# Performance work log

Hardware: AMD Instinct MI355X
Metric: run time of the kernel (lower is better)

## Reference

```python
import jax, jax.numpy as jnp
import numpy as np
import math

E = 2048         # n_embd
H = 16           # num query head pairs (num_heads)
HKV = 8          # num_kv_heads
NREP = H // HKV  # 2
HD = E // H // 2 # head_dim = 64
DEPTH = 12
LAMBDA_INIT = 0.8 - 0.6 * math.exp(-0.3 * DEPTH)
EPS = 1e-6


def setup_inputs() -> dict:
    key = jax.random.key(0)
    ks = jax.random.split(key, 10)
    s = lambda fan_in: 1.0 / np.sqrt(fan_in)
    return {
        "x": jax.random.normal(ks[0], (2, 2048, E), jnp.float32),
        "Wq": jax.random.normal(ks[1], (E, E), jnp.float32) * s(E),
        "Wk": jax.random.normal(ks[2], (E, E // NREP), jnp.float32) * s(E),
        "Wv": jax.random.normal(ks[3], (E, E // NREP), jnp.float32) * s(E),
        "Wo": jax.random.normal(ks[4], (E, E), jnp.float32) * s(E),
        "lam_q1": jax.random.normal(ks[5], (HD,), jnp.float32) * 0.1,
        "lam_k1": jax.random.normal(ks[6], (HD,), jnp.float32) * 0.1,
        "lam_q2": jax.random.normal(ks[7], (HD,), jnp.float32) * 0.1,
        "lam_k2": jax.random.normal(ks[8], (HD,), jnp.float32) * 0.1,
        "g": jnp.ones((2 * HD,), jnp.float32),  # RMSNorm weight
    }


def _rotary(x, cos, sin):
    # x: [B, T, nh, HD]; cos/sin: [T, HD//2]
    d = x.shape[-1] // 2
    x1, x2 = x[..., :d], x[..., d:]
    c = cos[None, :, None, :]
    si = sin[None, :, None, :]
    return jnp.concatenate([x1 * c + x2 * si, -x1 * si + x2 * c], axis=-1)


def reference(x, Wq, Wk, Wv, Wo, lam_q1, lam_k1, lam_q2, lam_k2, g):
    B, T, _ = x.shape
    q = (x @ Wq).reshape(B, T, 2 * H, HD)
    k = (x @ Wk).reshape(B, T, 2 * HKV, HD)
    v = (x @ Wv).reshape(B, T, HKV, 2 * HD)

    inv_freq = 1.0 / (10000.0 ** (jnp.arange(0, HD, 2, dtype=jnp.float32) / HD))
    freqs = jnp.arange(T, dtype=jnp.float32)[:, None] * inv_freq[None, :]
    cos, sin = jnp.cos(freqs), jnp.sin(freqs)
    q = _rotary(q, cos, sin)
    k = _rotary(k, cos, sin)

    q = jnp.transpose(q, (0, 2, 1, 3)) * (HD ** -0.5)   # [B, 2H, T, HD]
    k = jnp.repeat(jnp.transpose(k, (0, 2, 1, 3)), NREP, axis=1)  # [B, 2H, T, HD]
    v = jnp.repeat(jnp.transpose(v, (0, 2, 1, 3)), NREP, axis=1)  # [B, H, T, 2HD]

    scores = jnp.einsum('bhtd,bhsd->bhts', q, k)
    scores = jnp.nan_to_num(scores)
    mask = jnp.triu(jnp.full((T, T), -jnp.inf, scores.dtype), 1)
    scores = scores + mask
    p = jax.nn.softmax(scores.astype(jnp.float32), axis=-1).astype(scores.dtype)

    lam1 = jnp.exp(jnp.sum(lam_q1 * lam_k1))
    lam2 = jnp.exp(jnp.sum(lam_q2 * lam_k2))
    lam = lam1 - lam2 + LAMBDA_INIT

    p = p.reshape(B, H, 2, T, T)
    diff = p[:, :, 0] - lam * p[:, :, 1]               # [B, H, T, T]
    attn = jnp.einsum('bhts,bhsd->bhtd', diff, v)      # [B, H, T, 2HD]

    # RMSNorm over last dim (2*HD)
    attn = attn * jax.lax.rsqrt(jnp.mean(attn * attn, axis=-1, keepdims=True) + EPS) * g
    attn = attn * (1.0 - LAMBDA_INIT)
    attn = jnp.transpose(attn, (0, 2, 1, 3)).reshape(B, T, E)
    return attn @ Wo
```

## Files before the change

### kernel.cpp

```cpp
#include <hip/hip_runtime.h>

#define T_SEQ 2048

typedef __bf16 bf16x8 __attribute__((ext_vector_type(8)));
typedef float f32x4 __attribute__((ext_vector_type(4)));
typedef unsigned short u16;

__device__ __forceinline__ u16 f2b(float f) {
  unsigned u = __float_as_uint(f);
  unsigned r = 0x7fffu + ((u >> 16) & 1u);
  return (u16)((u + r) >> 16);
}
__device__ __forceinline__ float b2f(u16 v) {
  return __uint_as_float(((unsigned)v) << 16);
}
__device__ __forceinline__ f32x4 mfma16(bf16x8 a, bf16x8 b, f32x4 c) {
  return __builtin_amdgcn_mfma_f32_16x16x32_bf16(a, b, c, 0, 0, 0);
}
__device__ __forceinline__ unsigned pkhi(float lo, float hi) {
  return __builtin_amdgcn_perm(__float_as_uint(hi), __float_as_uint(lo), 0x07060302u);
}
#if defined(__has_builtin)
#if __has_builtin(__builtin_amdgcn_exp2f)
#define HAVE_RAW_EXP2 1
#endif
#endif
__device__ __forceinline__ float exp2r(float x) {
#ifdef HAVE_RAW_EXP2
  return __builtin_amdgcn_exp2f(x);
#else
  float r;
  asm("v_exp_f32 %0, %1" : "=v"(r) : "v"(x));
  return r;
#endif
}
__device__ __forceinline__ void glds16(const void* g, void* s) {
  __builtin_amdgcn_global_load_lds(
      (const __attribute__((address_space(1))) void*)(uintptr_t)g,
      (__attribute__((address_space(3))) void*)(unsigned)(uintptr_t)s, 16, 0, 0);
}

__global__ void lam_kernel(const float* __restrict__ q1, const float* __restrict__ k1,
                           const float* __restrict__ q2, const float* __restrict__ k2,
                           float* __restrict__ outp) {
  int l = threadIdx.x;
  float a = q1[l] * k1[l];
  float c = q2[l] * k2[l];
  #pragma unroll
  for (int off = 32; off > 0; off >>= 1) {
    a += __shfl_down(a, off);
    c += __shfl_down(c, off);
  }
  if (l == 0) outp[0] = expf(a) - expf(c) + 0.7836057665316244f;
}

__global__ __launch_bounds__(256) void convert_kernel(const float* __restrict__ in,
                                                      u16* __restrict__ outp, int n) {
  int i = (blockIdx.x * 256 + threadIdx.x) * 4;
  if (i >= n) return;
  float4 v = *(const float4*)(in + i);
  ushort4 pk;
  pk.x = f2b(v.x); pk.y = f2b(v.y); pk.z = f2b(v.z); pk.w = f2b(v.w);
  *(ushort4*)(outp + i) = pk;
}

__global__ __launch_bounds__(256) void transposeW_kernel(const float* __restrict__ Wq,
                                                         const float* __restrict__ Wk,
                                                         const float* __restrict__ Wv,
                                                         const float* __restrict__ Wo,
                                                         u16* __restrict__ outp) {
  __shared__ float tile[32][33];
  const int ro0 = blockIdx.y * 32;
  const int r0 = blockIdx.x * 32;
  const float* src; int C, cbase;
  if (ro0 < 2048)      { src = Wq; C = 2048; cbase = 0; }
  else if (ro0 < 3072) { src = Wk; C = 1024; cbase = 2048; }
  else if (ro0 < 4096) { src = Wv; C = 1024; cbase = 3072; }
  else                 { src = Wo; C = 2048; cbase = 4096; }
  const int cs0 = ro0 - cbase;
  const int tx = threadIdx.x & 31, ty = threadIdx.x >> 5;
  #pragma unroll
  for (int k2 = 0; k2 < 4; k2++)
    tile[ty * 4 + k2][tx] = src[(size_t)(r0 + ty * 4 + k2) * C + cs0 + tx];
  __syncthreads();
  #pragma unroll
  for (int k2 = 0; k2 < 4; k2++)
    outp[(size_t)(ro0 + ty * 4 + k2) * 2048 + r0 + tx] = f2b(tile[tx][ty * 4 + k2]);
}

template <bool OUT_BF16>
__global__ __launch_bounds__(256) void gemm128_kernel(const u16* __restrict__ A,
                                                      const u16* __restrict__ BT,
                                                      void* __restrict__ C, int N, int K) {
  __shared__ alignas(16) u16 As[128 * 64];
  __shared__ alignas(16) u16 Bs[128 * 64];
  const int tid = threadIdx.x, w = tid >> 6, lane = tid & 63;
  const int l15 = lane & 15, quad = lane >> 4;
  const int m0 = blockIdx.y * 128, n0 = blockIdx.x * 128;
  const int wm = (w >> 1) * 64, wn = (w & 1) * 64;
  const int lr = lane >> 3, slot = lane & 7, csw = slot ^ lr;
  f32x4 acc[4][4];
  #pragma unroll
  for (int mt = 0; mt < 4; mt++)
    #pragma unroll
    for (int nt = 0; nt < 4; nt++) acc[mt][nt] = (f32x4){0.f, 0.f, 0.f, 0.f};
  const u16* Ag = A + (size_t)(m0 + w * 32 + lr) * K + csw * 8;
  const u16* Bg = BT + (size_t)(n0 + w * 32 + lr) * K + csw * 8;
  u16* Asd = As + (w * 32) * 64;
  u16* Bsd = Bs + (w * 32) * 64;
  for (int kt = 0; kt < K; kt += 64) {
    #pragma unroll
    for (int i = 0; i < 4; i++) {
      glds16(Ag + kt + (size_t)(i * 8) * K, Asd + i * 512);
      glds16(Bg + kt + (size_t)(i * 8) * K, Bsd + i * 512);
    }
    __syncthreads();
    #pragma unroll
    for (int kk = 0; kk < 2; kk++) {
      bf16x8 am[4], bn[4];
      #pragma unroll
      for (int t = 0; t < 4; t++) {
        const int ra = wm + t * 16 + l15;
        am[t] = *(const bf16x8*)&As[ra * 64 + (((kk * 4 + quad) ^ (ra & 7)) << 3)];
        const int rb = wn + t * 16 + l15;
        bn[t] = *(const bf16x8*)&Bs[rb * 64 + (((kk * 4 + quad) ^ (rb & 7)) << 3)];
      }
      #pragma unroll
      for (int mt = 0; mt < 4; mt++)
        #pragma unroll
        for (int nt = 0; nt < 4; nt++) acc[mt][nt] = mfma16(am[mt], bn[nt], acc[mt][nt]);
    }
    __syncthreads();
  }
  const int row = m0 + wm + quad * 4;
  #pragma unroll
  for (int mt = 0; mt < 4; mt++) {
    #pragma unroll
    for (int nt = 0; nt < 4; nt++) {
      const int col = n0 + wn + nt * 16 + l15;
      #pragma unroll
      for (int rr = 0; rr < 4; rr++) {
        if (OUT_BF16)
          ((u16*)C)[(size_t)(row + mt * 16 + rr) * N + col] = f2b(acc[mt][nt][rr]);
        else
          ((float*)C)[(size_t)(row + mt * 16 + rr) * N + col] = acc[mt][nt][rr];
      }
    }
  }
}

#define STAGE_HALF(TILE, ROLE, BUF)                                                     \
  do {                                                                                  \
    const u16* sp_ = ((ROLE) == 0 || (ROLE) == 3 ? Ag : Bg) +                           \
                     (size_t)((ROLE) >= 2 ? 128 : 0) * K + (size_t)(TILE) * 64;         \
    u16* dp_ = ((ROLE) == 0 || (ROLE) == 3 ? &As[BUF][0] : &Bs[BUF][0]) +               \
               (((ROLE) >= 2 ? 128 : 0) + w * 8) * 64;                                  \
    glds16(sp_, dp_);                                                                   \
    glds16(sp_ + (size_t)64 * K, dp_ + 4096);                                           \
  } while (0)

#define PHASE(I, J, BUF, NEWA, NEWB, BN, STILE, SROLE, SBUF, DOVM)                      \
  do {                                                                                  \
    if (NEWA) {                                                                         \
      _Pragma("unroll") for (int u_ = 0; u_ < 4; u_++) {                                \
        const int ar_ = ((I) * 4 + u_) * 32 + wm * 16 + l15;                            \
        _Pragma("unroll") for (int kk_ = 0; kk_ < 2; kk_++)                             \
            am[u_][kk_] = *(const bf16x8*)&As[BUF][ar_ * 64 +                           \
                              (((kk_ * 4 + quad) ^ (ar_ & 7)) << 3)];                   \
      }                                                                                 \
    }                                                                                   \
    if (NEWB) {                                                                         \
      _Pragma("unroll") for (int v_ = 0; v_ < 2; v_++) {                                \
        const int br_ = ((J) * 2 + v_) * 64 + wn * 16 + l15;                            \
        _Pragma("unroll") for (int kk_ = 0; kk_ < 2; kk_++)                             \
            BN[v_][kk_] = *(const bf16x8*)&Bs[BUF][br_ * 64 +                           \
                              (((kk_ * 4 + quad) ^ (br_ & 7)) << 3)];                   \
      }                                                                                 \
    }                                                                                   \
    STAGE_HALF(STILE, SROLE, SBUF);                                                     \
    __builtin_amdgcn_s_barrier();                                                       \
    asm volatile("s_waitcnt lgkmcnt(0)" ::: "memory");                                  \
    __builtin_amdgcn_sched_barrier(0);                                                  \
    __builtin_amdgcn_s_setprio(1);                                                      \
    _Pragma("unroll") for (int u_ = 0; u_ < 4; u_++)                                    \
        _Pragma("unroll") for (int v_ = 0; v_ < 2; v_++) {                              \
      acc[(I) * 4 + u_][(J) * 2 + v_] =                                                 \
          mfma16(am[u_][0], BN[v_][0], acc[(I) * 4 + u_][(J) * 2 + v_]);                \
      acc[(I) * 4 + u_][(J) * 2 + v_] =                                                 \
          mfma16(am[u_][1], BN[v_][1], acc[(I) * 4 + u_][(J) * 2 + v_]);                \
    }                                                                                   \
    __builtin_amdgcn_s_setprio(0);                                                      \
    if (DOVM) asm volatile("s_waitcnt vmcnt(6)" ::: "memory");                          \
    __builtin_amdgcn_s_barrier();                                                       \
  } while (0)

__global__ __launch_bounds__(512, 2) void gemm256_kernel(const u16* __restrict__ A,
                                                         const u16* __restrict__ BT,
                                                         u16* __restrict__ C, int N, int K) {
  __shared__ alignas(16) u16 As[2][256 * 64];
  __shared__ alignas(16) u16 Bs[2][256 * 64];
  const int tid = threadIdx.x, w = tid >> 6, lane = tid & 63;
  const int l15 = lane & 15, quad = lane >> 4;
  const int wm = w >> 2, wn = w & 3;
  const int lr = lane >> 3, slot = lane & 7, csw = slot ^ lr;
  const int m0 = blockIdx.y * 256, n0 = blockIdx.x * 256;
  const int nkt = K >> 6;

  f32x4 acc[8][4];
  #pragma unroll
  for (int r = 0; r < 8; r++)
    #pragma unroll
    for (int s = 0; s < 4; s++) acc[r][s] = (f32x4){0.f, 0.f, 0.f, 0.f};

  const u16* Ag = A + (size_t)(m0 + w * 8 + lr) * K + csw * 8;
  const u16* Bg = BT + (size_t)(n0 + w * 8 + lr) * K + csw * 8;

  bf16x8 am[4][2], bn0[2][2], bn1[2][2];

  STAGE_HALF(0, 0, 0); STAGE_HALF(0, 1, 0); STAGE_HALF(0, 2, 0); STAGE_HALF(0, 3, 0);
  STAGE_HALF(1, 0, 1); STAGE_HALF(1, 1, 1); STAGE_HALF(1, 2, 1);
  asm volatile("s_waitcnt vmcnt(6)" ::: "memory");
  __builtin_amdgcn_s_barrier();

  #pragma unroll 1
  for (int t = 0; t < nkt; t += 2) {
    PHASE(0, 0, 0, 1, 1, bn0, t + 1, 3, 1, 0);
    PHASE(0, 1, 0, 0, 1, bn1, t + 2, 0, 0, 0);
    PHASE(1, 0, 0, 1, 0, bn0, t + 2, 1, 0, 0);
    PHASE(1, 1, 0, 0, 0, bn1, t + 2, 2, 0, 1);
    PHASE(0, 0, 1, 1, 1, bn0, t + 2, 3, 0, 0);
    PHASE(0, 1, 1, 0, 1, bn1, t + 3, 0, 1, 0);
    PHASE(1, 0, 1, 1, 0, bn0, t + 3, 1, 1, 0);
    PHASE(1, 1, 1, 0, 0, bn1, t + 3, 2, 1, 1);
  }

  const int crow = m0 + wm * 16 + quad * 4;
  const int ccol = n0 + wn * 16 + l15;
  #pragma unroll
  for (int r = 0; r < 8; r++)
    #pragma unroll
    for (int s = 0; s < 4; s++)
      #pragma unroll
      for (int rr = 0; rr < 4; rr++)
        C[(size_t)(crow + r * 32 + rr) * N + ccol + s * 64] = f2b(acc[r][s][rr]);
}

__global__ __launch_bounds__(256) void rotary_kernel(const u16* __restrict__ qkv,
                                                     u16* __restrict__ Qb,
                                                     u16* __restrict__ Kb, float qscale) {
  int idx = blockIdx.x * 256 + threadIdx.x;
  int i = idx & 31;
  int bt = (idx >> 5) & 4095;
  int hh = idx >> 17;
  int t = bt & (T_SEQ - 1), b = bt >> 11;
  bool isq = hh < 32;
  int col = isq ? hh * 64 : 2048 + (hh - 32) * 64;
  size_t inb = (size_t)bt * 4096 + col + i;
  float x1 = b2f(qkv[inb]);
  float x2 = b2f(qkv[inb + 32]);
  float invf = exp2f(-(float)i * 0.4152410118609203f);
  float ang = (float)t * invf;
  float c = cosf(ang), s = sinf(ang);
  float scale = isq ? qscale : 1.0f;
  float o1 = (x1 * c + x2 * s) * scale;
  float o2 = (x2 * c - x1 * s) * scale;
  u16* outp = isq ? (Qb + (size_t)(b * 32 + hh) * (T_SEQ * 64))
                  : (Kb + (size_t)(b * 16 + hh - 32) * (T_SEQ * 64));
  size_t ob = (size_t)t * 64 + i;
  outp[ob] = f2b(o1);
  outp[ob + 32] = f2b(o2);
}

__global__ __launch_bounds__(256) void vtrans_kernel(const u16* __restrict__ qkv,
                                                     u16* __restrict__ outp) {
  __shared__ unsigned tile[32][33];
  int bh = blockIdx.z;
  int t0 = blockIdx.x * 32, dv0 = blockIdx.y * 32;
  int tx = threadIdx.x & 31, ty = threadIdx.x >> 5;
  int bt_base = (bh >> 3) * T_SEQ;
  int col = 3072 + (bh & 7) * 128 + dv0 + tx;
  #pragma unroll
  for (int k2 = 0; k2 < 4; k2++)
    tile[ty * 4 + k2][tx] = qkv[(size_t)(bt_base + t0 + ty * 4 + k2) * 4096 + col];
  __syncthreads();
  const int stile = t0 >> 6;
  const int sold = (t0 & 63) + tx;
  const int slo = sold & 31, hb = sold >> 5;
  const int sp = hb * 32 + ((slo >> 2) & 3) * 8 + ((slo >> 4) & 1) * 4 + (slo & 3);
  #pragma unroll
  for (int k2 = 0; k2 < 4; k2++) {
    int dv = dv0 + ty * 4 + k2;
    outp[(((size_t)bh * 32 + stile) * 128 + dv) * 64 + sp] = (u16)tile[tx][ty * 4 + k2];
  }
}

__global__ __launch_bounds__(256) void attn_kernel(const u16* __restrict__ Qb,
                                                   const u16* __restrict__ Kb,
                                                   const u16* __restrict__ Vt,
                                                   const float* __restrict__ lamp,
                                                   const float* __restrict__ g,
                                                   u16* __restrict__ attn_out) {
  __shared__ alignas(16) char smem[49152];
  u16* const Ks0 = (u16*)smem;
  u16* const Vs0 = (u16*)(smem + 16384);
  u16* const Psb = (u16*)smem;
  const int pr = blockIdx.x;
  const int bh = blockIdx.y;
  const int b = bh >> 4, h = bh & 15;
  const int tid = threadIdx.x, w = tid >> 6, lane = tid & 63;
  const int l15 = lane & 15, quad = lane >> 4;
  const int lr = lane >> 3, slot = lane & 7, csw = slot ^ lr;
  const float lam = lamp[0];

  const u16* Kg = Kb + (size_t)(b * 16 + h) * (T_SEQ * 64) + (w * 16 + lr) * 64 + csw * 8;
  const u16* Vg = Vt + (size_t)(b * 8 + (h >> 1)) * (T_SEQ * 128) + w * 2048 + lr * 64 + csw * 8;
  u16* kd[2] = {Ks0 + w * 1024, Ks0 + 4096 + w * 1024};
  u16* vd[2] = {Vs0 + w * 2048, Vs0 + 8192 + w * 2048};

  #pragma unroll 1
  for (int half = 0; half < 2; half++) {
    const int tt = half ? 31 - pr : pr;
    const int qb = tt * 64 + w * 16;
    const int qglob = qb + l15;

    bf16x8 qf[2][2];
    #pragma unroll
    for (int e = 0; e < 2; e++)
      #pragma unroll
      for (int kk = 0; kk < 2; kk++)
        qf[e][kk] = *(const bf16x8*)&Qb[((size_t)(b * 32 + 2 * h + e) * T_SEQ + qb + l15) * 64 +
                                        kk * 32 + quad * 8];

    f32x4 o[2][8];
    float lsum[2] = {0.f, 0.f};
    #pragma unroll
    for (int e = 0; e < 2; e++)
      #pragma unroll
      for (int nt = 0; nt < 8; nt++) o[e][nt] = (f32x4){0.f, 0.f, 0.f, 0.f};

    glds16(Kg, kd[0]); glds16(Kg + 512, kd[0] + 512);
    glds16(Vg, vd[0]); glds16(Vg + 512, vd[0] + 512);
    glds16(Vg + 1024, vd[0] + 1024); glds16(Vg + 1536, vd[0] + 1536);

    #pragma unroll 1
    for (int st = 0; st <= tt; st++) {
      const int buf = st & 1;
      const u16* Ksb = Ks0 + buf * 4096;
      const u16* Vsb = Vs0 + buf * 8192;
      if (st < tt) {
        const u16* kp = Kg + (size_t)(st + 1) * 4096;
        const u16* vp = Vg + (size_t)(st + 1) * 8192;
        glds16(kp, kd[buf ^ 1]); glds16(kp + 512, kd[buf ^ 1] + 512);
        glds16(vp, vd[buf ^ 1]); glds16(vp + 512, vd[buf ^ 1] + 512);
        glds16(vp + 1024, vd[buf ^ 1] + 1024); glds16(vp + 1536, vd[buf ^ 1] + 1536);
        asm volatile("s_waitcnt vmcnt(6)" ::: "memory");
      } else {
        asm volatile("s_waitcnt vmcnt(0)" ::: "memory");
      }
      __builtin_amdgcn_s_barrier();
      __builtin_amdgcn_sched_barrier(0);

      bf16x8 kf[4][2];
      #pragma unroll
      for (int j = 0; j < 4; j++) {
        const int rk = j * 16 + l15;
        #pragma unroll
        for (int kk = 0; kk < 2; kk++)
          kf[j][kk] = *(const bf16x8*)&Ksb[rk * 64 + (((kk * 4 + quad) ^ (rk & 7)) << 3)];
      }

      bf16x8 pa[2][2];
      #pragma unroll
      for (int e = 0; e < 2; e++) {
        f32x4 sc[4];
        __builtin_amdgcn_s_setprio(1);
        #pragma unroll
        for (int j = 0; j < 4; j++) {
          f32x4 z = {0.f, 0.f, 0.f, 0.f};
          z = mfma16(kf[j][0], qf[e][0], z);
          sc[j] = mfma16(kf[j][1], qf[e][1], z);
        }
        __builtin_amdgcn_s_setprio(0);
        if (st == tt) {
          #pragma unroll
          for (int j = 0; j < 4; j++) {
            int srow = st * 64 + j * 16 + quad * 4;
            #pragma unroll
            for (int rr = 0; rr < 4; rr++)
              if (srow + rr > qglob) sc[j][rr] = -1e30f;
          }
        }
        float ls = 0.f;
        union { unsigned u[8]; bf16x8 v[2]; } pk;
        #pragma unroll
        for (int j = 0; j < 4; j++) {
          #pragma unroll
          for (int rr = 0; rr < 4; rr++) {
            float p = exp2r(sc[j][rr]);
            sc[j][rr] = p;
            ls += p;
          }
          pk.u[j * 2] = pkhi(sc[j][0], sc[j][1]);
          pk.u[j * 2 + 1] = pkhi(sc[j][2], sc[j][3]);
        }
        pa[e][0] = pk.v[0];
        pa[e][1] = pk.v[1];
        lsum[e] += ls;
      }
      __builtin_amdgcn_s_setprio(1);
      #pragma unroll
      for (int nt = 0; nt < 8; nt++) {
        const int rv = nt * 16 + l15;
        bf16x8 vf0 = *(const bf16x8*)&Vsb[rv * 64 + ((quad ^ (rv & 7)) << 3)];
        bf16x8 vf1 = *(const bf16x8*)&Vsb[rv * 64 + (((4 + quad) ^ (rv & 7)) << 3)];
        o[0][nt] = mfma16(vf0, pa[0][0], o[0][nt]);
        o[0][nt] = mfma16(vf1, pa[0][1], o[0][nt]);
        o[1][nt] = mfma16(vf0, pa[1][0], o[1][nt]);
        o[1][nt] = mfma16(vf1, pa[1][1], o[1][nt]);
      }
      __builtin_amdgcn_s_setprio(0);
      __builtin_amdgcn_s_barrier();
    }

    float l0 = lsum[0], l1 = lsum[1];
    l0 += __shfl_xor(l0, 16); l0 += __shfl_xor(l0, 32);
    l1 += __shfl_xor(l1, 16); l1 += __shfl_xor(l1, 32);
    const float il0 = 1.f / l0, il1 = lam / l1;
    float ssq = 0.f;
    #pragma unroll
    for (int nt = 0; nt < 8; nt++)
      #pragma unroll
      for (int rr = 0; rr < 4; rr++) {
        float v = o[0][nt][rr] * il0 - o[1][nt][rr] * il1;
        o[0][nt][rr] = v;
        ssq += v * v;
      }
    ssq += __shfl_xor(ssq, 16);
    ssq += __shfl_xor(ssq, 32);
    const float rsc = rsqrtf(ssq * (1.f / 128.f) + 1e-6f) * 0.2163942334683756f;
    #pragma unroll
    for (int nt = 0; nt < 8; nt++) {
      float4 gv = *(const float4*)&g[nt * 16 + quad * 4];
      uint2 pk;
      pk.x = (unsigned)f2b(o[0][nt][0] * rsc * gv.x) |
             ((unsigned)f2b(o[0][nt][1] * rsc * gv.y) << 16);
      pk.y = (unsigned)f2b(o[0][nt][2] * rsc * gv.z) |
             ((unsigned)f2b(o[0][nt][3] * rsc * gv.w) << 16);
      *(uint2*)&Psb[(w * 16 + l15) * 136 + nt * 16 + quad * 4] = pk;
    }
    asm volatile("s_waitcnt lgkmcnt(0)" ::: "memory");
    __builtin_amdgcn_sched_barrier(0);
    #pragma unroll
    for (int i = 0; i < 4; i++) {
      const int r = (lane >> 4) + i * 4, c = (lane & 15) * 8;
      bf16x8 ov = *(const bf16x8*)&Psb[(w * 16 + r) * 136 + c];
      *(bf16x8*)&attn_out[(size_t)(b * T_SEQ + qb + r) * 2048 + h * 128 + c] = ov;
    }
    __syncthreads();
  }
}

extern "C" void kernel_launch(void* const* d_in, const int* in_sizes, int n_in, void* d_out,
                              int out_size, void* d_ws, size_t ws_size, hipStream_t stream) {
  const float* x = (const float*)d_in[0];
  const float* Wq = (const float*)d_in[1];
  const float* Wk = (const float*)d_in[2];
  const float* Wv = (const float*)d_in[3];
  const float* Wo = (const float*)d_in[4];
  const float* lq1 = (const float*)d_in[5];
  const float* lk1 = (const float*)d_in[6];
  const float* lq2 = (const float*)d_in[7];
  const float* lk2 = (const float*)d_in[8];
  const float* g = (const float*)d_in[9];

  char* ws = (char*)d_ws;
  u16* WT = (u16*)(ws);
  u16* xbf = (u16*)(ws + 25165824);
  u16* QKV = (u16*)(ws + 41943040);
  u16* Qb = (u16*)(ws + 75497472);
  u16* Kb = (u16*)(ws + 92274688);
  u16* Vt = (u16*)(ws + 100663296);
  u16* Attn = (u16*)(ws + 109051904);
  float* lam = (float*)(ws + 125829120);

  lam_kernel<<<1, 64, 0, stream>>>(lq1, lk1, lq2, lk2, lam);
  convert_kernel<<<8192, 256, 0, stream>>>(x, xbf, 8388608);
  transposeW_kernel<<<dim3(64, 192), 256, 0, stream>>>(Wq, Wk, Wv, Wo, WT);
  gemm256_kernel<<<dim3(16, 16), 512, 0, stream>>>(xbf, WT, QKV, 4096, 2048);
  rotary_kernel<<<24576, 256, 0, stream>>>(QKV, Qb, Kb, 0.18033688011112042f);
  vtrans_kernel<<<dim3(64, 4, 16), 256, 0, stream>>>(QKV, Vt);
  attn_kernel<<<dim3(16, 32), 256, 0, stream>>>(Qb, Kb, Vt, lam, g, Attn);
  gemm128_kernel<false><<<dim3(16, 32), 256, 0, stream>>>(Attn, WT + (size_t)4096 * 2048, d_out,
                                                          2048, 2048);
}
```

Before: 337.7 us.

## Use 512-thread attention blocks covering 128 queries with shared KV tiles

The attention kernel moves from 256-thread blocks, each handling two 64-query tiles one after the other (paired for causal balance), to 512-thread blocks that handle one 128-query tile. Each K/V tile loaded into LDS is now shared by 8 waves instead of 4, halving global-to-LDS traffic per query, and each wave issues half as many loads. The grid is flattened to 512 blocks, ordered longest-first for the first half to balance the causal load, and the mask check runs whenever the step reaches the wave's own diagonal tile. The cost is that waves in the lower 64 rows do one fully masked extra KV step, and blocks are larger with higher register pressure under launch_bounds(512,4).

```diff
diff --git a/kernel.cpp b/kernel.cpp
--- a/kernel.cpp
+++ b/kernel.cpp
@@ -294,169 +294,166 @@
   }
 }
 
-__global__ __launch_bounds__(256) void attn_kernel(const u16* __restrict__ Qb,
-                                                   const u16* __restrict__ Kb,
-                                                   const u16* __restrict__ Vt,
-                                                   const float* __restrict__ lamp,
-                                                   const float* __restrict__ g,
-                                                   u16* __restrict__ attn_out) {
+__global__ __launch_bounds__(512, 4) void attn_kernel(const u16* __restrict__ Qb,
+                                                      const u16* __restrict__ Kb,
+                                                      const u16* __restrict__ Vt,
+                                                      const float* __restrict__ lamp,
+                                                      const float* __restrict__ g,
+                                                      u16* __restrict__ attn_out) {
   __shared__ alignas(16) char smem[49152];
   u16* const Ks0 = (u16*)smem;
   u16* const Vs0 = (u16*)(smem + 16384);
   u16* const Psb = (u16*)smem;
-  const int pr = blockIdx.x;
-  const int bh = blockIdx.y;
+  const int id = blockIdx.x;
+  const int araw = id & 15;
+  const int bh = (id >> 4) & 31;
+  const int a = (id < 256) ? 15 - araw : araw;
   const int b = bh >> 4, h = bh & 15;
   const int tid = threadIdx.x, w = tid >> 6, lane = tid & 63;
   const int l15 = lane & 15, quad = lane >> 4;
   const int lr = lane >> 3, slot = lane & 7, csw = slot ^ lr;
   const float lam = lamp[0];
 
-  const u16* Kg = Kb + (size_t)(b * 16 + h) * (T_SEQ * 64) + (w * 16 + lr) * 64 + csw * 8;
-  const u16* Vg = Vt + (size_t)(b * 8 + (h >> 1)) * (T_SEQ * 128) + w * 2048 + lr * 64 + csw * 8;
-  u16* kd[2] = {Ks0 + w * 1024, Ks0 + 4096 + w * 1024};
-  u16* vd[2] = {Vs0 + w * 2048, Vs0 + 8192 + w * 2048};
+  const int tlast = 2 * a + 1;
+  const int myTile = 2 * a + (w >> 2);
+  const int qb = a * 128 + w * 16;
+  const int qglob = qb + l15;
+
+  const u16* Kg = Kb + (size_t)(b * 16 + h) * (T_SEQ * 64) + (w * 8 + lr) * 64 + csw * 8;
+  const u16* Vg = Vt + (size_t)(b * 8 + (h >> 1)) * (T_SEQ * 128) + w * 1024 + lr * 64 + csw * 8;
+  u16* kd[2] = {Ks0 + w * 512, Ks0 + 4096 + w * 512};
+  u16* vd[2] = {Vs0 + w * 1024, Vs0 + 8192 + w * 1024};
+
+  bf16x8 qf[2][2];
+  #pragma unroll
+  for (int e = 0; e < 2; e++)
+    #pragma unroll
+    for (int kk = 0; kk < 2; kk++)
+      qf[e][kk] = *(const bf16x8*)&Qb[((size_t)(b * 32 + 2 * h + e) * T_SEQ + qb + l15) * 64 +
+                                      kk * 32 + quad * 8];
+
+  f32x4 o[2][8];
+  float lsum[2] = {0.f, 0.f};
+  #pragma unroll
+  for (int e = 0; e < 2; e++)
+    #pragma unroll
+    for (int nt = 0; nt < 8; nt++) o[e][nt] = (f32x4){0.f, 0.f, 0.f, 0.f};
+
+  glds16(Kg, kd[0]);
+  glds16(Vg, vd[0]); glds16(Vg + 512, vd[0] + 512);
 
   #pragma unroll 1
-  for (int half = 0; half < 2; half++) {
-    const int tt = half ? 31 - pr : pr;
-    const int qb = tt * 64 + w * 16;
-    const int qglob = qb + l15;
-
-    bf16x8 qf[2][2];
-    #pragma unroll
-    for (int e = 0; e < 2; e++)
+  for (int st = 0; st <= tlast; st++) {
+    const int buf = st & 1;
+    const u16* Ksb = Ks0 + buf * 4096;
+    const u16* Vsb = Vs0 + buf * 8192;
+    if (st < tlast) {
+      const u16* kp = Kg + (size_t)(st + 1) * 4096;
+      const u16* vp = Vg + (size_t)(st + 1) * 8192;
+      glds16(kp, kd[buf ^ 1]);
+      glds16(vp, vd[buf ^ 1]); glds16(vp + 512, vd[buf ^ 1] + 512);
+      asm volatile("s_waitcnt vmcnt(3)" ::: "memory");
+    } else {
+      asm volatile("s_waitcnt vmcnt(0)" ::: "memory");
+    }
+    __builtin_amdgcn_s_barrier();
+    __builtin_amdgcn_sched_barrier(0);
+
+    bf16x8 kf[4][2];
+    #pragma unroll
+    for (int j = 0; j < 4; j++) {
+      const int rk = j * 16 + l15;
       #pragma unroll
       for (int kk = 0; kk < 2; kk++)
-        qf[e][kk] = *(const bf16x8*)&Qb[((size_t)(b * 32 + 2 * h + e) * T_SEQ + qb + l15) * 64 +
-                                        kk * 32 + quad * 8];
-
-    f32x4 o[2][8];
-    float lsum[2] = {0.f, 0.f};
-    #pragma unroll
-    for (int e = 0; e < 2; e++)
-      #pragma unroll
-      for (int nt = 0; nt < 8; nt++) o[e][nt] = (f32x4){0.f, 0.f, 0.f, 0.f};
-
-    glds16(Kg, kd[0]); glds16(Kg + 512, kd[0] + 512);
-    glds16(Vg, vd[0]); glds16(Vg + 512, vd[0] + 512);
-    glds16(Vg + 1024, vd[0] + 1024); glds16(Vg + 1536, vd[0] + 1536);
-
-    #pragma unroll 1
-    for (int st = 0; st <= tt; st++) {
-      const int buf = st & 1;
-      const u16* Ksb = Ks0 + buf * 4096;
-      const u16* Vsb = Vs0 + buf * 8192;
-      if (st < tt) {
-        const u16* kp = Kg + (size_t)(st + 1) * 4096;
-        const u16* vp = Vg + (size_t)(st + 1) * 8192;
-        glds16(kp, kd[buf ^ 1]); glds16(kp + 512, kd[buf ^ 1] + 512);
-        glds16(vp, vd[buf ^ 1]); glds16(vp + 512, vd[buf ^ 1] + 512);
-        glds16(vp + 1024, vd[buf ^ 1] + 1024); glds16(vp + 1536, vd[buf ^ 1] + 1536);
-        asm volatile("s_waitcnt vmcnt(6)" ::: "memory");
-      } else {
-        asm volatile("s_waitcnt vmcnt(0)" ::: "memory");
+        kf[j][kk] = *(const bf16x8*)&Ksb[rk * 64 + (((kk * 4 + quad) ^ (rk & 7)) << 3)];
+    }
+
+    bf16x8 pa[2][2];
+    #pragma unroll
+    for (int e = 0; e < 2; e++) {
+      f32x4 sc[4];
+      __builtin_amdgcn_s_setprio(1);
+      #pragma unroll
+      for (int j = 0; j < 4; j++) {
+        f32x4 z = {0.f, 0.f, 0.f, 0.f};
+        z = mfma16(kf[j][0], qf[e][0], z);
+        sc[j] = mfma16(kf[j][1], qf[e][1], z);
       }
-      __builtin_amdgcn_s_barrier();
-      __builtin_amdgcn_sched_barrier(0);
-
-      bf16x8 kf[4][2];
-      #pragma unroll
-      for (int j = 0; j < 4; j++) {
-        const int rk = j * 16 + l15;
-        #pragma unroll
-        for (int kk = 0; kk < 2; kk++)
-          kf[j][kk] = *(const bf16x8*)&Ksb[rk * 64 + (((kk * 4 + quad) ^ (rk & 7)) << 3)];
-      }
-
-      bf16x8 pa[2][2];
-      #pragma unroll
-      for (int e = 0; e < 2; e++) {
-        f32x4 sc[4];
-        __builtin_amdgcn_s_setprio(1);
+      __builtin_amdgcn_s_setprio(0);
+      if (st >= myTile) {
         #pragma unroll
         for (int j = 0; j < 4; j++) {
-          f32x4 z = {0.f, 0.f, 0.f, 0.f};
-          z = mfma16(kf[j][0], qf[e][0], z);
-          sc[j] = mfma16(kf[j][1], qf[e][1], z);
+          int srow = st * 64 + j * 16 + quad * 4;
+          #pragma unroll
+          for (int rr = 0; rr < 4; rr++)
+            if (srow + rr > qglob) sc[j][rr] = -1e30f;
         }
-        __builtin_amdgcn_s_setprio(0);
-        if (st == tt) {
-          #pragma unroll
-          for (int j = 0; j < 4; j++) {
-            int srow = st * 64 + j * 16 + quad * 4;
-            #pragma unroll
-            for (int rr = 0; rr < 4; rr++)
-              if (srow + rr > qglob) sc[j][rr] = -1e30f;
-          }
+      }
+      float ls = 0.f;
+      union { unsigned u[8]; bf16x8 v[2]; } pk;
+      #pragma unroll
+      for (int j = 0; j < 4; j++) {
+        #pragma unroll
+        for (int rr = 0; rr < 4; rr++) {
+          float p = exp2r(sc[j][rr]);
+          sc[j][rr] = p;
+          ls += p;
         }
-        float ls = 0.f;
-        union { unsigned u[8]; bf16x8 v[2]; } pk;
-        #pragma unroll
-        for (int j = 0; j < 4; j++) {
-          #pragma unroll
-          for (int rr = 0; rr < 4; rr++) {
-            float p = exp2r(sc[j][rr]);
-            sc[j][rr] = p;
-            ls += p;
-          }
-          pk.u[j * 2] = pkhi(sc[j][0], sc[j][1]);
-          pk.u[j * 2 + 1] = pkhi(sc[j][2], sc[j][3]);
-        }
-        pa[e][0] = pk.v[0];
-        pa[e][1] = pk.v[1];
-        lsum[e] += ls;
+        pk.u[j * 2] = pkhi(sc[j][0], sc[j][1]);
+        pk.u[j * 2 + 1] = pkhi(sc[j][2], sc[j][3]);
       }
-      __builtin_amdgcn_s_setprio(1);
-      #pragma unroll
-      for (int nt = 0; nt < 8; nt++) {
-        const int rv = nt * 16 + l15;
-        bf16x8 vf0 = *(const bf16x8*)&Vsb[rv * 64 + ((quad ^ (rv & 7)) << 3)];
-        bf16x8 vf1 = *(const bf16x8*)&Vsb[rv * 64 + (((4 + quad) ^ (rv & 7)) << 3)];
-        o[0][nt] = mfma16(vf0, pa[0][0], o[0][nt]);
-        o[0][nt] = mfma16(vf1, pa[0][1], o[0][nt]);
-        o[1][nt] = mfma16(vf0, pa[1][0], o[1][nt]);
-        o[1][nt] = mfma16(vf1, pa[1][1], o[1][nt]);
-      }
-      __builtin_amdgcn_s_setprio(0);
-      __builtin_amdgcn_s_barrier();
-    }
-
-    float l0 = lsum[0], l1 = lsum[1];
-    l0 += __shfl_xor(l0, 16); l0 += __shfl_xor(l0, 32);
-    l1 += __shfl_xor(l1, 16); l1 += __shfl_xor(l1, 32);
-    const float il0 = 1.f / l0, il1 = lam / l1;
-    float ssq = 0.f;
-    #pragma unroll
-    for (int nt = 0; nt < 8; nt++)
-      #pragma unroll
-      for (int rr = 0; rr < 4; rr++) {
-        float v = o[0][nt][rr] * il0 - o[1][nt][rr] * il1;
-        o[0][nt][rr] = v;
-        ssq += v * v;
-      }
-    ssq += __shfl_xor(ssq, 16);
-    ssq += __shfl_xor(ssq, 32);
-    const float rsc = rsqrtf(ssq * (1.f / 128.f) + 1e-6f) * 0.2163942334683756f;
+      pa[e][0] = pk.v[0];
+      pa[e][1] = pk.v[1];
+      lsum[e] += ls;
+    }
+    __builtin_amdgcn_s_setprio(1);
     #pragma unroll
     for (int nt = 0; nt < 8; nt++) {
-      float4 gv = *(const float4*)&g[nt * 16 + quad * 4];
-      uint2 pk;
-      pk.x = (unsigned)f2b(o[0][nt][0] * rsc * gv.x) |
-             ((unsigned)f2b(o[0][nt][1] * rsc * gv.y) << 16);
-      pk.y = (unsigned)f2b(o[0][nt][2] * rsc * gv.z) |
-             ((unsigned)f2b(o[0][nt][3] * rsc * gv.w) << 16);
-      *(uint2*)&Psb[(w * 16 + l15) * 136 + nt * 16 + quad * 4] = pk;
-    }
-    asm volatile("s_waitcnt lgkmcnt(0)" ::: "memory");
-    __builtin_amdgcn_sched_barrier(0);
-    #pragma unroll
-    for (int i = 0; i < 4; i++) {
-      const int r = (lane >> 4) + i * 4, c = (lane & 15) * 8;
-      bf16x8 ov = *(const bf16x8*)&Psb[(w * 16 + r) * 136 + c];
-      *(bf16x8*)&attn_out[(size_t)(b * T_SEQ + qb + r) * 2048 + h * 128 + c] = ov;
-    }
-    __syncthreads();
+      const int rv = nt * 16 + l15;
+      bf16x8 vf0 = *(const bf16x8*)&Vsb[rv * 64 + ((quad ^ (rv & 7)) << 3)];
+      bf16x8 vf1 = *(const bf16x8*)&Vsb[rv * 64 + (((4 + quad) ^ (rv & 7)) << 3)];
+      o[0][nt] = mfma16(vf0, pa[0][0], o[0][nt]);
+      o[0][nt] = mfma16(vf1, pa[0][1], o[0][nt]);
+      o[1][nt] = mfma16(vf0, pa[1][0], o[1][nt]);
+      o[1][nt] = mfma16(vf1, pa[1][1], o[1][nt]);
+    }
+    __builtin_amdgcn_s_setprio(0);
+    __builtin_amdgcn_s_barrier();
+  }
+
+  float l0 = lsum[0], l1 = lsum[1];
+  l0 += __shfl_xor(l0, 16); l0 += __shfl_xor(l0, 32);
+  l1 += __shfl_xor(l1, 16); l1 += __shfl_xor(l1, 32);
+  const float il0 = 1.f / l0, il1 = lam / l1;
+  float ssq = 0.f;
+  #pragma unroll
+  for (int nt = 0; nt < 8; nt++)
+    #pragma unroll
+    for (int rr = 0; rr < 4; rr++) {
+      float v = o[0][nt][rr] * il0 - o[1][nt][rr] * il1;
+      o[0][nt][rr] = v;
+      ssq += v * v;
+    }
+  ssq += __shfl_xor(ssq, 16);
+  ssq += __shfl_xor(ssq, 32);
+  const float rsc = rsqrtf(ssq * (1.f / 128.f) + 1e-6f) * 0.2163942334683756f;
+  #pragma unroll
+  for (int nt = 0; nt < 8; nt++) {
+    float4 gv = *(const float4*)&g[nt * 16 + quad * 4];
+    uint2 pk;
+    pk.x = (unsigned)f2b(o[0][nt][0] * rsc * gv.x) |
+           ((unsigned)f2b(o[0][nt][1] * rsc * gv.y) << 16);
+    pk.y = (unsigned)f2b(o[0][nt][2] * rsc * gv.z) |
+           ((unsigned)f2b(o[0][nt][3] * rsc * gv.w) << 16);
+    *(uint2*)&Psb[(w * 16 + l15) * 136 + nt * 16 + quad * 4] = pk;
+  }
+  asm volatile("s_waitcnt lgkmcnt(0)" ::: "memory");
+  __builtin_amdgcn_sched_barrier(0);
+  #pragma unroll
+  for (int i = 0; i < 4; i++) {
+    const int r = (lane >> 4) + i * 4, c = (lane & 15) * 8;
+    bf16x8 ov = *(const bf16x8*)&Psb[(w * 16 + r) * 136 + c];
+    *(bf16x8*)&attn_out[(size_t)(b * T_SEQ + qb + r) * 2048 + h * 128 + c] = ov;
   }
 }
 
@@ -489,7 +486,7 @@
   gemm256_kernel<<<dim3(16, 16), 512, 0, stream>>>(xbf, WT, QKV, 4096, 2048);
   rotary_kernel<<<24576, 256, 0, stream>>>(QKV, Qb, Kb, 0.18033688011112042f);
   vtrans_kernel<<<dim3(64, 4, 16), 256, 0, stream>>>(QKV, Vt);
-  attn_kernel<<<dim3(16, 32), 256, 0, stream>>>(Qb, Kb, Vt, lam, g, Attn);
+  attn_kernel<<<512, 512, 0, stream>>>(Qb, Kb, Vt, lam, g, Attn);
   gemm128_kernel<false><<<dim3(16, 32), 256, 0, stream>>>(Attn, WT + (size_t)4096 * 2048, d_out,
                                                           2048, 2048);
 }
```

New measurement: 487.7 us. 44.4% more time.
